# Kernel tuning notes

Measured on AMD Instinct MI355X. Metric: run time of the kernel, lower is better.

The kernel has to match this reference:

```python
import jax, jax.numpy as jnp
from jax import lax
import numpy as np
import math

N = 8
IN_CH = 3
EPS = 1e-6


def _dct_basis(n=N):
    # basis[u, i] = c(u) * cos(pi * u * (i + 0.5) / n)
    u = np.arange(n)
    i = np.arange(n)
    b = np.cos(np.pi * np.outer(u, i + 0.5) / n)
    c = np.full(n, math.sqrt(2.0 / n))
    c[0] = math.sqrt(1.0 / n)
    return b * c[:, None]


def _dct_conv_weight(n=N, in_ch=IN_CH):
    # weight[k = u*n + v, i, j] = basis[u,i] * basis[v,j]; grouped conv OIHW with I=1
    b = _dct_basis(n)
    w = np.einsum('ui,vj->uvij', b, b).reshape(n * n, 1, n, n).astype(np.float32)
    return np.concatenate([w] * in_ch, axis=0)  # [in_ch*n*n, 1, n, n]


def setup_inputs() -> dict:
    key = jax.random.key(0)
    k1, k2, k3 = jax.random.split(key, 3)
    B, C, H, W = 32, 3, 512, 512
    x = jax.random.uniform(k1, (B, C, H, W), dtype=jnp.float32)  # RGB in [0,1)
    # per-(sample, channel) stats; keep divisor d = max - min + eps > 1 so the
    # B-times repeated in-place normalization of the original stays finite
    max_ = 1.5 + jax.random.uniform(k2, (B, C * N * N, 1, 1), dtype=jnp.float32)
    min_ = 0.1 * jax.random.uniform(k3, (B, C * N * N, 1, 1), dtype=jnp.float32)
    ycbcr_w = jnp.asarray(
        [[0.299, 0.587, 0.114],
         [-0.169, -0.331, 0.5],
         [0.5, -0.419, -0.081]], dtype=jnp.float32)  # [out_c, in_c]
    dct_w = jnp.asarray(_dct_conv_weight())  # [192, 1, 8, 8]
    return {"x": x, "max_": max_, "min_": min_, "ycbcr_w": ycbcr_w, "dct_w": dct_w}


def reference(x, max_, min_, ycbcr_w, dct_w):
    # 1x1 RGB -> YCbCr conv == channel matmul
    ycbcr = jnp.einsum('oc,bchw->bohw', ycbcr_w, x)
    # grouped 8x8 stride-8 block-DCT conv: [B, 192, H/8, W/8]
    dct = lax.conv_general_dilated(
        ycbcr, dct_w, window_strides=(N, N), padding='VALID',
        feature_group_count=IN_CH,
        dimension_numbers=('NCHW', 'OIHW', 'NCHW'))
    # Original applies t = (t - min) / (max - min + eps) in-place B times per
    # sample (outer loop index i is unused but repeats the whole inner loop).
    d = max_ - min_ + EPS
    B = x.shape[0]
    out = lax.fori_loop(0, B, lambda i, t: (t - min_) / d, dct)
    return out
```

## Files before the change

kernel.cpp:

```cpp
#include <hip/hip_runtime.h>


#define HW 512
#define CHST (HW * HW)
#define NPAIR 6144
#define EPS 1e-6f

static constexpr float BASIS[8][8] = {
  { 0.35355339059327373f, 0.35355339059327373f, 0.35355339059327373f, 0.35355339059327373f,
    0.35355339059327373f, 0.35355339059327373f, 0.35355339059327373f, 0.35355339059327373f },
  { 0.49039264020161522f, 0.41573480615127262f, 0.27778511650980114f, 0.09754516100806412f,
   -0.09754516100806412f,-0.27778511650980114f,-0.41573480615127262f,-0.49039264020161522f },
  { 0.46193976625564337f, 0.19134171618254492f,-0.19134171618254492f,-0.46193976625564337f,
   -0.46193976625564337f,-0.19134171618254492f, 0.19134171618254492f, 0.46193976625564337f },
  { 0.41573480615127262f,-0.09754516100806412f,-0.49039264020161522f,-0.27778511650980114f,
    0.27778511650980114f, 0.49039264020161522f, 0.09754516100806412f,-0.41573480615127262f },
  { 0.35355339059327373f,-0.35355339059327373f,-0.35355339059327373f, 0.35355339059327373f,
    0.35355339059327373f,-0.35355339059327373f,-0.35355339059327373f, 0.35355339059327373f },
  { 0.27778511650980114f,-0.49039264020161522f, 0.09754516100806412f, 0.41573480615127262f,
   -0.41573480615127262f,-0.09754516100806412f, 0.49039264020161522f,-0.27778511650980114f },
  { 0.19134171618254492f,-0.46193976625564337f, 0.46193976625564337f,-0.19134171618254492f,
   -0.19134171618254492f, 0.46193976625564337f,-0.46193976625564337f, 0.19134171618254492f },
  { 0.09754516100806412f,-0.27778511650980114f, 0.41573480615127262f,-0.49039264020161522f,
    0.49039264020161522f,-0.41573480615127262f, 0.27778511650980114f,-0.09754516100806412f }
};

__global__ void precomp_norm(const float* __restrict__ max_,
                             const float* __restrict__ min_,
                             float* __restrict__ so) {
    int i = blockIdx.x * 256 + threadIdx.x;
    if (i >= NPAIR) return;
    float mn = min_[i], mx = max_[i];
    float d = mx - mn + EPS;
    float a = 1.0f / d;
    float a2 = a * a, a4 = a2 * a2, a8 = a4 * a4, a16 = a8 * a8, a32 = a16 * a16;
    float geo = a * (1.0f - a32) / (1.0f - a);
    so[2 * i]     = a32;
    so[2 * i + 1] = -mn * geo;
}

template <bool USE_WS>
__global__ __launch_bounds__(192)
void dct_kernel(const float* __restrict__ x,
                const float* __restrict__ ycbcr_w,
                const float* __restrict__ so,
                const float* __restrict__ max_,
                const float* __restrict__ min_,
                float* __restrict__ out) {
    const int b  = blockIdx.x >> 6;
    const int by = blockIdx.x & 63;
    const int c  = threadIdx.x >> 6;
    const int bx = threadIdx.x & 63;

    const float w0 = ycbcr_w[c * 3 + 0];
    const float w1 = ycbcr_w[c * 3 + 1];
    const float w2 = ycbcr_w[c * 3 + 2];

    const float* x0 = x + (size_t)(b * 3) * CHST + (by * 8) * HW + bx * 8;

    float tmp[8][8];
#pragma unroll
    for (int u = 0; u < 8; ++u)
#pragma unroll
        for (int j = 0; j < 8; ++j) tmp[u][j] = 0.0f;

#pragma unroll
    for (int i = 0; i < 8; ++i) {
        const float* r = x0 + i * HW;
        float R[8], G[8], Bl[8];
        *(float4*)(&R[0])  = *(const float4*)(r);
        *(float4*)(&R[4])  = *(const float4*)(r + 4);
        *(float4*)(&G[0])  = *(const float4*)(r + CHST);
        *(float4*)(&G[4])  = *(const float4*)(r + CHST + 4);
        *(float4*)(&Bl[0]) = *(const float4*)(r + 2 * CHST);
        *(float4*)(&Bl[4]) = *(const float4*)(r + 2 * CHST + 4);
        float y[8];
#pragma unroll
        for (int j = 0; j < 8; ++j)
            y[j] = fmaf(w0, R[j], fmaf(w1, G[j], w2 * Bl[j]));
#pragma unroll
        for (int u = 0; u < 8; ++u) {
            const float bu = BASIS[u][i];
#pragma unroll
            for (int j = 0; j < 8; ++j)
                tmp[u][j] = fmaf(bu, y[j], tmp[u][j]);
        }
    }

    const int obase = b * 192 + c * 64;
    float* op = out + ((size_t)obase * 64 + by) * 64 + bx;

#pragma unroll
    for (int u = 0; u < 8; ++u) {
#pragma unroll
        for (int v = 0; v < 8; ++v) {
            float acc = tmp[u][0] * BASIS[v][0];
#pragma unroll
            for (int j = 1; j < 8; ++j)
                acc = fmaf(tmp[u][j], BASIS[v][j], acc);
            const int k = u * 8 + v;
            float s, o;
            if (USE_WS) {
                s = so[(obase + k) * 2];
                o = so[(obase + k) * 2 + 1];
            } else {
                float mn = min_[obase + k], mx = max_[obase + k];
                float d  = mx - mn + EPS;
                float a  = 1.0f / d;
                float a2 = a * a, a4 = a2 * a2, a8 = a4 * a4, a16 = a8 * a8, a32 = a16 * a16;
                s = a32;
                o = -mn * (a * (1.0f - a32) / (1.0f - a));
            }
            op[(size_t)k * 4096] = fmaf(s, acc, o);
        }
    }
}

extern "C" void kernel_launch(void* const* d_in, const int* in_sizes, int n_in,
                              void* d_out, int out_size, void* d_ws, size_t ws_size,
                              hipStream_t stream) {
    const float* x    = (const float*)d_in[0];
    const float* max_ = (const float*)d_in[1];
    const float* min_ = (const float*)d_in[2];
    const float* yw   = (const float*)d_in[3];
    float* out = (float*)d_out;
    float* so  = (float*)d_ws;

    const bool use_ws = (ws_size >= (size_t)NPAIR * 2 * sizeof(float));
    if (use_ws) {
        precomp_norm<<<(NPAIR + 255) / 256, 256, 0, stream>>>(max_, min_, so);
        dct_kernel<true><<<32 * 64, 192, 0, stream>>>(x, yw, so, max_, min_, out);
    } else {
        dct_kernel<false><<<32 * 64, 192, 0, stream>>>(x, yw, nullptr, max_, min_, out);
    }
}
```

Before: 197.6 us.

## Stage coalesced RGB band loads through LDS before per-block DCT

Each block now loads its full 8-row band of R, G and B with fully coalesced float4 reads across 256 threads, computes YCbCr once per pixel, and writes the three Y planes into 48KB of shared memory. After a barrier, 192 threads each read their 8x8 block from LDS and run the separable DCT as before. This replaces the strided per-thread 32-byte global reads of the original, which had poor coalescing. The cost is 48KB of LDS per block, which limits occupancy, plus one barrier and 64 idle threads during the DCT phase.

```diff
diff --git a/kernel.cpp b/kernel.cpp
--- a/kernel.cpp
+++ b/kernel.cpp
@@ -40,78 +40,108 @@
 }
 
 template <bool USE_WS>
-__global__ __launch_bounds__(192)
+__global__ __launch_bounds__(256)
 void dct_kernel(const float* __restrict__ x,
                 const float* __restrict__ ycbcr_w,
                 const float* __restrict__ so,
                 const float* __restrict__ max_,
                 const float* __restrict__ min_,
                 float* __restrict__ out) {
+    __shared__ float ylds[3 * 8 * HW];
+
     const int b  = blockIdx.x >> 6;
     const int by = blockIdx.x & 63;
-    const int c  = threadIdx.x >> 6;
-    const int bx = threadIdx.x & 63;
+    const int t  = threadIdx.x;
 
-    const float w0 = ycbcr_w[c * 3 + 0];
-    const float w1 = ycbcr_w[c * 3 + 1];
-    const float w2 = ycbcr_w[c * 3 + 2];
+    const float* band = x + (size_t)(b * 3) * CHST + (by * 8) * HW;
 
-    const float* x0 = x + (size_t)(b * 3) * CHST + (by * 8) * HW + bx * 8;
+    float w00 = ycbcr_w[0], w01 = ycbcr_w[1], w02 = ycbcr_w[2];
+    float w10 = ycbcr_w[3], w11 = ycbcr_w[4], w12 = ycbcr_w[5];
+    float w20 = ycbcr_w[6], w21 = ycbcr_w[7], w22 = ycbcr_w[8];
 
-    float tmp[8][8];
+    float4 Rv[4], Gv[4], Bv[4];
 #pragma unroll
-    for (int u = 0; u < 8; ++u)
+    for (int w = 0; w < 4; ++w) {
+        const int o = t + 256 * w;
+        Rv[w] = ((const float4*)(band))[o];
+        Gv[w] = ((const float4*)(band + CHST))[o];
+        Bv[w] = ((const float4*)(band + 2 * CHST))[o];
+    }
+    float4* yv = (float4*)ylds;
 #pragma unroll
-        for (int j = 0; j < 8; ++j) tmp[u][j] = 0.0f;
+    for (int w = 0; w < 4; ++w) {
+        const int o = t + 256 * w;
+        float4 y0, y1, y2;
+        y0.x = fmaf(w00, Rv[w].x, fmaf(w01, Gv[w].x, w02 * Bv[w].x));
+        y0.y = fmaf(w00, Rv[w].y, fmaf(w01, Gv[w].y, w02 * Bv[w].y));
+        y0.z = fmaf(w00, Rv[w].z, fmaf(w01, Gv[w].z, w02 * Bv[w].z));
+        y0.w = fmaf(w00, Rv[w].w, fmaf(w01, Gv[w].w, w02 * Bv[w].w));
+        y1.x = fmaf(w10, Rv[w].x, fmaf(w11, Gv[w].x, w12 * Bv[w].x));
+        y1.y = fmaf(w10, Rv[w].y, fmaf(w11, Gv[w].y, w12 * Bv[w].y));
+        y1.z = fmaf(w10, Rv[w].z, fmaf(w11, Gv[w].z, w12 * Bv[w].z));
+        y1.w = fmaf(w10, Rv[w].w, fmaf(w11, Gv[w].w, w12 * Bv[w].w));
+        y2.x = fmaf(w20, Rv[w].x, fmaf(w21, Gv[w].x, w22 * Bv[w].x));
+        y2.y = fmaf(w20, Rv[w].y, fmaf(w21, Gv[w].y, w22 * Bv[w].y));
+        y2.z = fmaf(w20, Rv[w].z, fmaf(w21, Gv[w].z, w22 * Bv[w].z));
+        y2.w = fmaf(w20, Rv[w].w, fmaf(w21, Gv[w].w, w22 * Bv[w].w));
+        yv[o]          = y0;
+        yv[1024 + o]   = y1;
+        yv[2048 + o]   = y2;
+    }
+    __syncthreads();
+
+    if (t < 192) {
+        const int c  = t >> 6;
+        const int bx = t & 63;
+
+        const float* yl = ylds + c * (8 * HW) + bx * 8;
+
+        float tmp[8][8];
+#pragma unroll
+        for (int u = 0; u < 8; ++u)
+#pragma unroll
+            for (int j = 0; j < 8; ++j) tmp[u][j] = 0.0f;
 
 #pragma unroll
-    for (int i = 0; i < 8; ++i) {
-        const float* r = x0 + i * HW;
-        float R[8], G[8], Bl[8];
-        *(float4*)(&R[0])  = *(const float4*)(r);
-        *(float4*)(&R[4])  = *(const float4*)(r + 4);
-        *(float4*)(&G[0])  = *(const float4*)(r + CHST);
-        *(float4*)(&G[4])  = *(const float4*)(r + CHST + 4);
-        *(float4*)(&Bl[0]) = *(const float4*)(r + 2 * CHST);
-        *(float4*)(&Bl[4]) = *(const float4*)(r + 2 * CHST + 4);
-        float y[8];
+        for (int i = 0; i < 8; ++i) {
+            float y[8];
+            *(float4*)(&y[0]) = *(const float4*)(yl + i * HW);
+            *(float4*)(&y[4]) = *(const float4*)(yl + i * HW + 4);
 #pragma unroll
-        for (int j = 0; j < 8; ++j)
-            y[j] = fmaf(w0, R[j], fmaf(w1, G[j], w2 * Bl[j]));
+            for (int u = 0; u < 8; ++u) {
+                const float bu = BASIS[u][i];
+#pragma unroll
+                for (int j = 0; j < 8; ++j)
+                    tmp[u][j] = fmaf(bu, y[j], tmp[u][j]);
+            }
+        }
+
+        const int obase = b * 192 + c * 64;
+        float* op = out + ((size_t)obase * 64 + by) * 64 + bx;
+
 #pragma unroll
         for (int u = 0; u < 8; ++u) {
-            const float bu = BASIS[u][i];
 #pragma unroll
-            for (int j = 0; j < 8; ++j)
-                tmp[u][j] = fmaf(bu, y[j], tmp[u][j]);
-        }
-    }
-
-    const int obase = b * 192 + c * 64;
-    float* op = out + ((size_t)obase * 64 + by) * 64 + bx;
-
+            for (int v = 0; v < 8; ++v) {
+                float acc = tmp[u][0] * BASIS[v][0];
 #pragma unroll
-    for (int u = 0; u < 8; ++u) {
-#pragma unroll
-        for (int v = 0; v < 8; ++v) {
-            float acc = tmp[u][0] * BASIS[v][0];
-#pragma unroll
-            for (int j = 1; j < 8; ++j)
-                acc = fmaf(tmp[u][j], BASIS[v][j], acc);
-            const int k = u * 8 + v;
-            float s, o;
-            if (USE_WS) {
-                s = so[(obase + k) * 2];
-                o = so[(obase + k) * 2 + 1];
-            } else {
-                float mn = min_[obase + k], mx = max_[obase + k];
-                float d  = mx - mn + EPS;
-                float a  = 1.0f / d;
-                float a2 = a * a, a4 = a2 * a2, a8 = a4 * a4, a16 = a8 * a8, a32 = a16 * a16;
-                s = a32;
-                o = -mn * (a * (1.0f - a32) / (1.0f - a));
+                for (int j = 1; j < 8; ++j)
+                    acc = fmaf(tmp[u][j], BASIS[v][j], acc);
+                const int k = u * 8 + v;
+                float s, o;
+                if (USE_WS) {
+                    s = so[(obase + k) * 2];
+                    o = so[(obase + k) * 2 + 1];
+                } else {
+                    float mn = min_[obase + k], mx = max_[obase + k];
+                    float d  = mx - mn + EPS;
+                    float a  = 1.0f / d;
+                    float a2 = a * a, a4 = a2 * a2, a8 = a4 * a4, a16 = a8 * a8, a32 = a16 * a16;
+                    s = a32;
+                    o = -mn * (a * (1.0f - a32) / (1.0f - a));
+                }
+                op[(size_t)k * 4096] = fmaf(s, acc, o);
             }
-            op[(size_t)k * 4096] = fmaf(s, acc, o);
         }
     }
 }
@@ -129,8 +159,8 @@
     const bool use_ws = (ws_size >= (size_t)NPAIR * 2 * sizeof(float));
     if (use_ws) {
         precomp_norm<<<(NPAIR + 255) / 256, 256, 0, stream>>>(max_, min_, so);
-        dct_kernel<true><<<32 * 64, 192, 0, stream>>>(x, yw, so, max_, min_, out);
+        dct_kernel<true><<<32 * 64, 256, 0, stream>>>(x, yw, so, max_, min_, out);
     } else {
-        dct_kernel<false><<<32 * 64, 192, 0, stream>>>(x, yw, nullptr, max_, min_, out);
+        dct_kernel<false><<<32 * 64, 256, 0, stream>>>(x, yw, nullptr, max_, min_, out);
     }
 }
```

Measured after the change: 187.3 us. -5.2%, faster.

## Stage input rows into LDS with async global_load_lds in a persistent-grid loop

Applied to the files above, without the earlier changes.

The DCT kernel becomes persistent with 768 blocks looping over 2048 row bands. Each band's RGB rows are copied straight into a 48KB LDS buffer with global_load_lds, and the next band's load is issued before the current band's output writes so that reading and writing overlap. Per-thread global loads were 32-byte strided and are replaced by coalesced 16-byte lanes. In exchange the LDS use limits occupancy, each band now needs two block-wide barriers, and LDS reads at an 8-float stride per lane may hit bank conflicts.

```diff
diff --git a/kernel.cpp b/kernel.cpp
--- a/kernel.cpp
+++ b/kernel.cpp
@@ -3,8 +3,13 @@
 
 #define HW 512
 #define CHST (HW * HW)
+#define NBAND 2048
+#define GRID 768
 #define NPAIR 6144
 #define EPS 1e-6f
+
+#define GLOBAL_AS __attribute__((address_space(1)))
+#define LDS_AS    __attribute__((address_space(3)))
 
 static constexpr float BASIS[8][8] = {
   { 0.35355339059327373f, 0.35355339059327373f, 0.35355339059327373f, 0.35355339059327373f,
@@ -47,72 +52,101 @@
                 const float* __restrict__ max_,
                 const float* __restrict__ min_,
                 float* __restrict__ out) {
-    const int b  = blockIdx.x >> 6;
-    const int by = blockIdx.x & 63;
-    const int c  = threadIdx.x >> 6;
-    const int bx = threadIdx.x & 63;
+    __shared__ float ylds[3 * 8 * HW];
 
-    const float w0 = ycbcr_w[c * 3 + 0];
-    const float w1 = ycbcr_w[c * 3 + 1];
-    const float w2 = ycbcr_w[c * 3 + 2];
+    const int t    = threadIdx.x;
+    const int w    = t >> 6;
+    const int lane = t & 63;
 
-    const float* x0 = x + (size_t)(b * 3) * CHST + (by * 8) * HW + bx * 8;
+    const float w0 = ycbcr_w[w * 3 + 0];
+    const float w1 = ycbcr_w[w * 3 + 1];
+    const float w2 = ycbcr_w[w * 3 + 2];
 
-    float tmp[8][8];
+    auto prefetch = [&](int m) {
+        const int b  = m >> 6;
+        const int by = m & 63;
+        const float* g0 = x + ((size_t)(b * 3 + w)) * CHST + (size_t)(by * 8) * HW + lane * 4;
+        float* l0 = ylds + w * 4096;
 #pragma unroll
-    for (int u = 0; u < 8; ++u)
+        for (int k = 0; k < 16; ++k) {
+            __builtin_amdgcn_global_load_lds(
+                (const GLOBAL_AS void*)(g0 + k * 256),
+                (LDS_AS void*)(l0 + k * 256), 16, 0, 0);
+        }
+    };
+
+    const int m0 = blockIdx.x;
+    prefetch(m0);
+    __syncthreads();
+
+    for (int m = m0; m < NBAND; m += GRID) {
+        const int b  = m >> 6;
+        const int by = m & 63;
+        const int bx = lane;
+
+        const float* rl = ylds + bx * 8;
+        const float* gl = rl + 4096;
+        const float* bl = rl + 8192;
+
+        float tmp[8][8];
 #pragma unroll
-        for (int j = 0; j < 8; ++j) tmp[u][j] = 0.0f;
+        for (int u = 0; u < 8; ++u)
+#pragma unroll
+            for (int j = 0; j < 8; ++j) tmp[u][j] = 0.0f;
 
 #pragma unroll
-    for (int i = 0; i < 8; ++i) {
-        const float* r = x0 + i * HW;
-        float R[8], G[8], Bl[8];
-        *(float4*)(&R[0])  = *(const float4*)(r);
-        *(float4*)(&R[4])  = *(const float4*)(r + 4);
-        *(float4*)(&G[0])  = *(const float4*)(r + CHST);
-        *(float4*)(&G[4])  = *(const float4*)(r + CHST + 4);
-        *(float4*)(&Bl[0]) = *(const float4*)(r + 2 * CHST);
-        *(float4*)(&Bl[4]) = *(const float4*)(r + 2 * CHST + 4);
-        float y[8];
+        for (int i = 0; i < 8; ++i) {
+            float R[8], G[8], Bl[8], y[8];
+            *(float4*)(&R[0])  = *(const float4*)(rl + i * HW);
+            *(float4*)(&R[4])  = *(const float4*)(rl + i * HW + 4);
+            *(float4*)(&G[0])  = *(const float4*)(gl + i * HW);
+            *(float4*)(&G[4])  = *(const float4*)(gl + i * HW + 4);
+            *(float4*)(&Bl[0]) = *(const float4*)(bl + i * HW);
+            *(float4*)(&Bl[4]) = *(const float4*)(bl + i * HW + 4);
 #pragma unroll
-        for (int j = 0; j < 8; ++j)
-            y[j] = fmaf(w0, R[j], fmaf(w1, G[j], w2 * Bl[j]));
+            for (int j = 0; j < 8; ++j)
+                y[j] = fmaf(w0, R[j], fmaf(w1, G[j], w2 * Bl[j]));
+#pragma unroll
+            for (int u = 0; u < 8; ++u) {
+                const float bu = BASIS[u][i];
+#pragma unroll
+                for (int j = 0; j < 8; ++j)
+                    tmp[u][j] = fmaf(bu, y[j], tmp[u][j]);
+            }
+        }
+        __syncthreads();
+
+        if (m + GRID < NBAND) prefetch(m + GRID);
+
+        const int obase = b * 192 + w * 64;
+        float* op = out + ((size_t)obase * 64 + by) * 64 + bx;
+
 #pragma unroll
         for (int u = 0; u < 8; ++u) {
-            const float bu = BASIS[u][i];
 #pragma unroll
-            for (int j = 0; j < 8; ++j)
-                tmp[u][j] = fmaf(bu, y[j], tmp[u][j]);
+            for (int v = 0; v < 8; ++v) {
+                float acc = tmp[u][0] * BASIS[v][0];
+#pragma unroll
+                for (int j = 1; j < 8; ++j)
+                    acc = fmaf(tmp[u][j], BASIS[v][j], acc);
+                const int k = u * 8 + v;
+                float s, o;
+                if (USE_WS) {
+                    s = so[(obase + k) * 2];
+                    o = so[(obase + k) * 2 + 1];
+                } else {
+                    float mn = min_[obase + k], mx = max_[obase + k];
+                    float d  = mx - mn + EPS;
+                    float a  = 1.0f / d;
+                    float a2 = a * a, a4 = a2 * a2, a8 = a4 * a4, a16 = a8 * a8, a32 = a16 * a16;
+                    s = a32;
+                    o = -mn * (a * (1.0f - a32) / (1.0f - a));
+                }
+                op[(size_t)k * 4096] = fmaf(s, acc, o);
+            }
         }
-    }
 
-    const int obase = b * 192 + c * 64;
-    float* op = out + ((size_t)obase * 64 + by) * 64 + bx;
-
-#pragma unroll
-    for (int u = 0; u < 8; ++u) {
-#pragma unroll
-        for (int v = 0; v < 8; ++v) {
-            float acc = tmp[u][0] * BASIS[v][0];
-#pragma unroll
-            for (int j = 1; j < 8; ++j)
-                acc = fmaf(tmp[u][j], BASIS[v][j], acc);
-            const int k = u * 8 + v;
-            float s, o;
-            if (USE_WS) {
-                s = so[(obase + k) * 2];
-                o = so[(obase + k) * 2 + 1];
-            } else {
-                float mn = min_[obase + k], mx = max_[obase + k];
-                float d  = mx - mn + EPS;
-                float a  = 1.0f / d;
-                float a2 = a * a, a4 = a2 * a2, a8 = a4 * a4, a16 = a8 * a8, a32 = a16 * a16;
-                s = a32;
-                o = -mn * (a * (1.0f - a32) / (1.0f - a));
-            }
-            op[(size_t)k * 4096] = fmaf(s, acc, o);
-        }
+        __syncthreads();
     }
 }
 
@@ -129,8 +163,8 @@
     const bool use_ws = (ws_size >= (size_t)NPAIR * 2 * sizeof(float));
     if (use_ws) {
         precomp_norm<<<(NPAIR + 255) / 256, 256, 0, stream>>>(max_, min_, so);
-        dct_kernel<true><<<32 * 64, 192, 0, stream>>>(x, yw, so, max_, min_, out);
+        dct_kernel<true><<<GRID, 192, 0, stream>>>(x, yw, so, max_, min_, out);
     } else {
-        dct_kernel<false><<<32 * 64, 192, 0, stream>>>(x, yw, nullptr, max_, min_, out);
+        dct_kernel<false><<<GRID, 192, 0, stream>>>(x, yw, nullptr, max_, min_, out);
     }
 }
```

After: 189.5 us. -4.1%, faster.

## Stage YCbCr band in LDS and split DCT rows across waves

Applied to the files above, without the earlier changes.

Each block now loads its 8-row band of all three RGB channels with coalesced float4 reads, computes all three YCbCr channels in registers, and stages one channel at a time in shared memory. Four waves each compute two of the eight DCT row frequencies for every 8x8 block in the band, instead of one thread doing a full 8x8 DCT. This aims to remove the strided per-thread global loads, the threefold re-reading of RGB per output channel, and the large per-thread register array. In exchange it adds LDS traffic, extra __syncthreads, and redundant LDS reads of the band by each wave.

```diff
diff --git a/kernel.cpp b/kernel.cpp
--- a/kernel.cpp
+++ b/kernel.cpp
@@ -39,65 +39,39 @@
     so[2 * i + 1] = -mn * geo;
 }
 
-template <bool USE_WS>
-__global__ __launch_bounds__(192)
-void dct_kernel(const float* __restrict__ x,
-                const float* __restrict__ ycbcr_w,
-                const float* __restrict__ so,
-                const float* __restrict__ max_,
-                const float* __restrict__ min_,
-                float* __restrict__ out) {
-    const int b  = blockIdx.x >> 6;
-    const int by = blockIdx.x & 63;
-    const int c  = threadIdx.x >> 6;
-    const int bx = threadIdx.x & 63;
-
-    const float w0 = ycbcr_w[c * 3 + 0];
-    const float w1 = ycbcr_w[c * 3 + 1];
-    const float w2 = ycbcr_w[c * 3 + 2];
-
-    const float* x0 = x + (size_t)(b * 3) * CHST + (by * 8) * HW + bx * 8;
-
-    float tmp[8][8];
+template <int U0, bool USE_WS>
+__device__ __forceinline__
+void dct_cols(const float* __restrict__ ylds, int lane, int obase, int by,
+              const float* __restrict__ so, const float* __restrict__ max_,
+              const float* __restrict__ min_, float* __restrict__ out) {
+    const float* yb = ylds + lane * 8;
+    float t0[8], t1[8];
 #pragma unroll
-    for (int u = 0; u < 8; ++u)
-#pragma unroll
-        for (int j = 0; j < 8; ++j) tmp[u][j] = 0.0f;
+    for (int j = 0; j < 8; ++j) { t0[j] = 0.0f; t1[j] = 0.0f; }
 
 #pragma unroll
     for (int i = 0; i < 8; ++i) {
-        const float* r = x0 + i * HW;
-        float R[8], G[8], Bl[8];
-        *(float4*)(&R[0])  = *(const float4*)(r);
-        *(float4*)(&R[4])  = *(const float4*)(r + 4);
-        *(float4*)(&G[0])  = *(const float4*)(r + CHST);
-        *(float4*)(&G[4])  = *(const float4*)(r + CHST + 4);
-        *(float4*)(&Bl[0]) = *(const float4*)(r + 2 * CHST);
-        *(float4*)(&Bl[4]) = *(const float4*)(r + 2 * CHST + 4);
-        float y[8];
+        float yv[8];
+        *(float4*)(&yv[0]) = *(const float4*)(yb + i * HW);
+        *(float4*)(&yv[4]) = *(const float4*)(yb + i * HW + 4);
+        const float b0 = BASIS[U0][i];
+        const float b1 = BASIS[U0 + 1][i];
 #pragma unroll
-        for (int j = 0; j < 8; ++j)
-            y[j] = fmaf(w0, R[j], fmaf(w1, G[j], w2 * Bl[j]));
-#pragma unroll
-        for (int u = 0; u < 8; ++u) {
-            const float bu = BASIS[u][i];
-#pragma unroll
-            for (int j = 0; j < 8; ++j)
-                tmp[u][j] = fmaf(bu, y[j], tmp[u][j]);
+        for (int j = 0; j < 8; ++j) {
+            t0[j] = fmaf(b0, yv[j], t0[j]);
+            t1[j] = fmaf(b1, yv[j], t1[j]);
         }
     }
 
-    const int obase = b * 192 + c * 64;
-    float* op = out + ((size_t)obase * 64 + by) * 64 + bx;
+    float* op = out + ((size_t)obase * 64 + by) * 64 + lane;
 
-#pragma unroll
-    for (int u = 0; u < 8; ++u) {
+    auto colpass = [&](const float (&tp)[8], int u) {
 #pragma unroll
         for (int v = 0; v < 8; ++v) {
-            float acc = tmp[u][0] * BASIS[v][0];
+            float acc = tp[0] * BASIS[v][0];
 #pragma unroll
             for (int j = 1; j < 8; ++j)
-                acc = fmaf(tmp[u][j], BASIS[v][j], acc);
+                acc = fmaf(tp[j], BASIS[v][j], acc);
             const int k = u * 8 + v;
             float s, o;
             if (USE_WS) {
@@ -113,7 +87,78 @@
             }
             op[(size_t)k * 4096] = fmaf(s, acc, o);
         }
+    };
+    colpass(t0, U0);
+    colpass(t1, U0 + 1);
+}
+
+template <bool USE_WS>
+__global__ __launch_bounds__(256, 5)
+void dct_kernel(const float* __restrict__ x,
+                const float* __restrict__ ycbcr_w,
+                const float* __restrict__ so,
+                const float* __restrict__ max_,
+                const float* __restrict__ min_,
+                float* __restrict__ out) {
+    __shared__ float ylds[8 * HW];
+
+    const int b    = blockIdx.x >> 6;
+    const int by   = blockIdx.x & 63;
+    const int t    = threadIdx.x;
+    const int wv   = t >> 6;
+    const int lane = t & 63;
+
+    const float* band = x + (size_t)(b * 3) * CHST + (size_t)(by * 8) * HW;
+
+    float4 Yv[4], Cbv[4], Crv[4];
+#pragma unroll
+    for (int q = 0; q < 4; ++q) {
+        const int o = t + 256 * q;
+        Yv[q]  = ((const float4*)(band))[o];
+        Cbv[q] = ((const float4*)(band + CHST))[o];
+        Crv[q] = ((const float4*)(band + 2 * CHST))[o];
     }
+    const float w00 = ycbcr_w[0], w01 = ycbcr_w[1], w02 = ycbcr_w[2];
+    const float w10 = ycbcr_w[3], w11 = ycbcr_w[4], w12 = ycbcr_w[5];
+    const float w20 = ycbcr_w[6], w21 = ycbcr_w[7], w22 = ycbcr_w[8];
+#pragma unroll
+    for (int q = 0; q < 4; ++q) {
+        const float4 r = Yv[q], g = Cbv[q], bb = Crv[q];
+        float4 y, cb, cr;
+        y.x  = fmaf(w00, r.x, fmaf(w01, g.x, w02 * bb.x));
+        y.y  = fmaf(w00, r.y, fmaf(w01, g.y, w02 * bb.y));
+        y.z  = fmaf(w00, r.z, fmaf(w01, g.z, w02 * bb.z));
+        y.w  = fmaf(w00, r.w, fmaf(w01, g.w, w02 * bb.w));
+        cb.x = fmaf(w10, r.x, fmaf(w11, g.x, w12 * bb.x));
+        cb.y = fmaf(w10, r.y, fmaf(w11, g.y, w12 * bb.y));
+        cb.z = fmaf(w10, r.z, fmaf(w11, g.z, w12 * bb.z));
+        cb.w = fmaf(w10, r.w, fmaf(w11, g.w, w12 * bb.w));
+        cr.x = fmaf(w20, r.x, fmaf(w21, g.x, w22 * bb.x));
+        cr.y = fmaf(w20, r.y, fmaf(w21, g.y, w22 * bb.y));
+        cr.z = fmaf(w20, r.z, fmaf(w21, g.z, w22 * bb.z));
+        cr.w = fmaf(w20, r.w, fmaf(w21, g.w, w22 * bb.w));
+        Yv[q] = y; Cbv[q] = cb; Crv[q] = cr;
+    }
+
+    float4* yv4 = (float4*)ylds;
+
+    auto round = [&](const float4 (&V)[4], int c, bool last) {
+#pragma unroll
+        for (int q = 0; q < 4; ++q) yv4[t + 256 * q] = V[q];
+        __syncthreads();
+        const int obase = b * 192 + c * 64;
+        switch (wv) {
+            case 0: dct_cols<0, USE_WS>(ylds, lane, obase, by, so, max_, min_, out); break;
+            case 1: dct_cols<2, USE_WS>(ylds, lane, obase, by, so, max_, min_, out); break;
+            case 2: dct_cols<4, USE_WS>(ylds, lane, obase, by, so, max_, min_, out); break;
+            default: dct_cols<6, USE_WS>(ylds, lane, obase, by, so, max_, min_, out); break;
+        }
+        if (!last) __syncthreads();
+    };
+
+    round(Yv,  0, false);
+    round(Cbv, 1, false);
+    round(Crv, 2, true);
 }
 
 extern "C" void kernel_launch(void* const* d_in, const int* in_sizes, int n_in,
@@ -129,8 +174,8 @@
     const bool use_ws = (ws_size >= (size_t)NPAIR * 2 * sizeof(float));
     if (use_ws) {
         precomp_norm<<<(NPAIR + 255) / 256, 256, 0, stream>>>(max_, min_, so);
-        dct_kernel<true><<<32 * 64, 192, 0, stream>>>(x, yw, so, max_, min_, out);
+        dct_kernel<true><<<32 * 64, 256, 0, stream>>>(x, yw, so, max_, min_, out);
     } else {
-        dct_kernel<false><<<32 * 64, 192, 0, stream>>>(x, yw, nullptr, max_, min_, out);
+        dct_kernel<false><<<32 * 64, 256, 0, stream>>>(x, yw, nullptr, max_, min_, out);
     }
 }
```

After: 189.7 us. 1.04x faster.
